# Performance work log

Hardware: AMD Instinct MI355X
Metric: run time of the kernel (lower is better)

The kernel has to match this reference:

```python
import jax, jax.numpy as jnp
import numpy as np

B, S, D, H = 4, 2048, 1024, 16
Dh = D // H


def _layernorm(x, a, b):
    # torch.var default is unbiased (ddof=1)
    mu = jnp.mean(x, axis=-1, keepdims=True)
    sg = jnp.var(x, axis=-1, keepdims=True, ddof=1)
    return (x - mu) / jnp.sqrt(sg + 1e-08) * a + b


def setup_inputs() -> dict:
    key = jax.random.key(0)
    ks = jax.random.split(key, 16)
    s = 1.0 / np.sqrt(D)
    inp = {
        'q': jax.random.normal(ks[0], (B, S, D), jnp.float32),
        'k': jax.random.normal(ks[1], (B, S, D), jnp.float32),
        'v': jax.random.normal(ks[2], (B, S, D), jnp.float32),
        'g': jax.random.normal(ks[3], (B, S, D), jnp.float32),
        # causal mask: True = masked
        'm': jnp.triu(jnp.ones((S, S), jnp.bool_), k=1)[None, None],
        'Wq': jax.random.uniform(ks[4], (D, D), jnp.float32, -s, s),
        'bq': jnp.zeros((D,), jnp.float32),
        'Wk': jax.random.uniform(ks[5], (D, D), jnp.float32, -s, s),
        'bk': jnp.zeros((D,), jnp.float32),
        'Wv': jax.random.uniform(ks[6], (D, D), jnp.float32, -s, s),
        'bv': jnp.zeros((D,), jnp.float32),
        'Wg': jax.random.uniform(ks[7], (D, D), jnp.float32, -s, s),
        'bg': jnp.zeros((D,), jnp.float32),
        'ln_a': jnp.ones((D,), jnp.float32),
        'ln_b': jnp.zeros((D,), jnp.float32),
        'Wo': jax.random.uniform(ks[8], (D, D), jnp.float32, -s, s),
        'bo': jnp.zeros((D,), jnp.float32),
    }
    return inp


def reference(q, k, v, g, m, Wq, bq, Wk, bk, Wv, bv, Wg, bg, ln_a, ln_b, Wo, bo):
    qp = q @ Wq.T + bq
    kp = k @ Wk.T + bk
    vp = v @ Wv.T + bv
    gp = g @ Wg.T + bg
    # gating path: exact GELU (torch default), then custom LayerNorm (unbiased var)
    vp = jax.nn.gelu(vp, approximate=False)
    gp = jax.nn.gelu(gp, approximate=False)
    vp = _layernorm(vp, ln_a, ln_b)
    # [B,S,D] -> [B,H,S,Dh]
    qh = qp.reshape(B, S, H, Dh).transpose(0, 2, 1, 3)
    kh = kp.reshape(B, S, H, Dh).transpose(0, 2, 1, 3)
    vh = vp.reshape(B, S, H, Dh).transpose(0, 2, 1, 3)
    gh = gp.reshape(B, S, H, Dh).transpose(0, 2, 1, 3)
    a = jnp.einsum('bhqd,bhkd->bhqk', qh, kh) / jnp.sqrt(jnp.float32(Dh))
    a = jnp.where(m, -jnp.inf, a)
    a = jax.nn.softmax(a, axis=-1)
    # dropout = 0.0 (inference): no-op
    o = jnp.einsum('bhqk,bhkd->bhqd', a, vh)
    o = o * gh
    o = o.transpose(0, 2, 1, 3).reshape(B, S, D)
    o = o @ Wo.T + bo
    return (o, a)
```

## Files before the change

kernel.cpp:

```cpp
#include <hip/hip_runtime.h>
#include <hip/hip_bf16.h>
#include <cstdint>
#include <cstddef>

#define DEVINL static __device__ __forceinline__

typedef short bf16x8 __attribute__((ext_vector_type(8)));
typedef short s16x4  __attribute__((ext_vector_type(4)));
typedef float f32x4  __attribute__((ext_vector_type(4)));
typedef unsigned short u16;

static constexpr int Bb = 4, Ss = 2048, Dd = 1024, Hh = 16;
static constexpr int Mrows = Bb * Ss;
static constexpr int BHc = Bb * Hh;

DEVINL u16 f2bf(float f) {
    union { float f; uint32_t u; } v; v.f = f;
    uint32_t r = v.u + 0x7fffu + ((v.u >> 16) & 1u);
    return (u16)(r >> 16);
}
DEVINL float bf2f(u16 h) {
    union { uint32_t u; float f; } v; v.u = ((uint32_t)h) << 16;
    return v.f;
}
DEVINL uint32_t cvt_pk_bf16(float lo, float hi) {
    uint32_t r;
    asm("v_cvt_pk_bf16_f32 %0, %1, %2" : "=v"(r) : "v"(lo), "v"(hi));
    return r;
}
DEVINL float gelu_exact(float x) {
    return 0.5f * x * (1.0f + erff(x * 0.70710678118654752f));
}
DEVINL void gload16(const u16* gsrc, u16* ldsdst) {
    auto* g = reinterpret_cast<const __attribute__((address_space(1))) uint32_t*>(
        reinterpret_cast<uintptr_t>(gsrc));
    auto* l = reinterpret_cast<__attribute__((address_space(3))) uint32_t*>(
        reinterpret_cast<uintptr_t>(ldsdst));
    __builtin_amdgcn_global_load_lds(g, l, 16, 0, 0);
}

__global__ __launch_bounds__(256) void k_cvt_in(
    const float* __restrict__ s0, const float* __restrict__ s1,
    const float* __restrict__ s2, const float* __restrict__ s3,
    u16* __restrict__ d0, u16* __restrict__ d1,
    u16* __restrict__ d2, u16* __restrict__ d3, int n4) {
    int t = blockIdx.x * 256 + threadIdx.x;
    if (t >= n4) return;
    const float* s; u16* d;
    switch (blockIdx.y) {
        case 0: s = s0; d = d0; break;
        case 1: s = s1; d = d1; break;
        case 2: s = s2; d = d2; break;
        default: s = s3; d = d3; break;
    }
    float4 v = ((const float4*)s)[t];
    ushort4 o;
    o.x = f2bf(v.x); o.y = f2bf(v.y); o.z = f2bf(v.z); o.w = f2bf(v.w);
    ((ushort4*)d)[t] = o;
}

__global__ __launch_bounds__(256) void k_cvt_w(
    const float* __restrict__ s0, const float* __restrict__ s1,
    const float* __restrict__ s2, const float* __restrict__ s3,
    const float* __restrict__ s4,
    u16* __restrict__ d0, u16* __restrict__ d1, u16* __restrict__ d2,
    u16* __restrict__ d3, u16* __restrict__ d4, int n4) {
    int t = blockIdx.x * 256 + threadIdx.x;
    if (t >= n4) return;
    const float* s; u16* d;
    switch (blockIdx.y) {
        case 0: s = s0; d = d0; break;
        case 1: s = s1; d = d1; break;
        case 2: s = s2; d = d2; break;
        case 3: s = s3; d = d3; break;
        default: s = s4; d = d4; break;
    }
    float4 v = ((const float4*)s)[t];
    ushort4 o;
    o.x = f2bf(v.x); o.y = f2bf(v.y); o.z = f2bf(v.z); o.w = f2bf(v.w);
    ((ushort4*)d)[t] = o;
}

__global__ __launch_bounds__(256, 3) void k_proj(
    const u16* __restrict__ qb, const u16* __restrict__ kb,
    const u16* __restrict__ vb, const u16* __restrict__ gb,
    const u16* __restrict__ Wqb, const u16* __restrict__ Wkb,
    const u16* __restrict__ Wvb, const u16* __restrict__ Wgb,
    const float* __restrict__ bqp, const float* __restrict__ bkp,
    const float* __restrict__ bvp, const float* __restrict__ bgp,
    u16* __restrict__ qp, u16* __restrict__ kpo,
    float* __restrict__ vp, u16* __restrict__ ghb)
{
    __shared__ u16 As[2][128 * 32];
    __shared__ u16 Bs[2][128 * 32];
    const int tid = threadIdx.x, lane = tid & 63, w = tid >> 6;
    const int wm = w >> 1, wn = w & 1;
    const int g = lane >> 4, li = lane & 15;
    const int orig = blockIdx.x;
    const int lid = (orig & 7) * 256 + (orig >> 3);
    const int z = lid >> 9, rem = lid & 511;
    const int m0 = (rem >> 3) * 128, n0 = (rem & 7) * 128;

    const u16 *Ap, *Wp; const float* bias;
    switch (z) {
        case 0: Ap = qb; Wp = Wqb; bias = bqp; break;
        case 1: Ap = kb; Wp = Wkb; bias = bkp; break;
        case 2: Ap = vb; Wp = Wvb; bias = bvp; break;
        default: Ap = gb; Wp = Wgb; bias = bgp; break;
    }

    const int ch0 = (w * 2 + 0) * 64 + lane, ch1 = (w * 2 + 1) * 64 + lane;
    const int row0 = ch0 >> 2, cp0 = ch0 & 3, row1 = ch1 >> 2, cp1 = ch1 & 3;
    const size_t aoff0 = (size_t)(m0 + row0) * 1024 + ((cp0 ^ ((row0 >> 1) & 3)) << 3);
    const size_t aoff1 = (size_t)(m0 + row1) * 1024 + ((cp1 ^ ((row1 >> 1) & 3)) << 3);
    const size_t boff0 = (size_t)(n0 + row0) * 1024 + ((cp0 ^ ((row0 >> 1) & 3)) << 3);
    const size_t boff1 = (size_t)(n0 + row1) * 1024 + ((cp1 ^ ((row1 >> 1) & 3)) << 3);
    const int ldst0 = (w * 2 + 0) * 512, ldst1 = (w * 2 + 1) * 512;

    const f32x4 zero4 = {0.f, 0.f, 0.f, 0.f};
    f32x4 acc[4][4];
#pragma unroll
    for (int m = 0; m < 4; m++)
#pragma unroll
        for (int n = 0; n < 4; n++) acc[m][n] = zero4;

    gload16(Ap + aoff0, &As[0][ldst0]);
    gload16(Ap + aoff1, &As[0][ldst1]);
    gload16(Wp + boff0, &Bs[0][ldst0]);
    gload16(Wp + boff1, &Bs[0][ldst1]);
    __syncthreads();

    for (int kt = 0; kt < 32; ++kt) {
        const int cur = kt & 1;
        if (kt < 31) {
            const int k0n = (kt + 1) * 32;
            gload16(Ap + aoff0 + k0n, &As[cur ^ 1][ldst0]);
            gload16(Ap + aoff1 + k0n, &As[cur ^ 1][ldst1]);
            gload16(Wp + boff0 + k0n, &Bs[cur ^ 1][ldst0]);
            gload16(Wp + boff1 + k0n, &Bs[cur ^ 1][ldst1]);
        }
        bf16x8 af[4], bfr[4];
#pragma unroll
        for (int m = 0; m < 4; m++) {
            int row = wm * 64 + m * 16 + li;
            af[m] = *(const bf16x8*)&As[cur][row * 32 + ((g ^ ((row >> 1) & 3)) << 3)];
        }
#pragma unroll
        for (int n = 0; n < 4; n++) {
            int row = wn * 64 + n * 16 + li;
            bfr[n] = *(const bf16x8*)&Bs[cur][row * 32 + ((g ^ ((row >> 1) & 3)) << 3)];
        }
#pragma unroll
        for (int m = 0; m < 4; m++)
#pragma unroll
            for (int n = 0; n < 4; n++)
                acc[m][n] = __builtin_amdgcn_mfma_f32_16x16x32_bf16(af[m], bfr[n], acc[m][n], 0, 0, 0);
        __syncthreads();
    }

#pragma unroll
    for (int m = 0; m < 4; m++) {
#pragma unroll
        for (int n = 0; n < 4; n++) {
            int col = n0 + wn * 64 + n * 16 + li;
            float bv = bias[col];
#pragma unroll
            for (int r = 0; r < 4; r++) {
                int row = m0 + wm * 64 + m * 16 + g * 4 + r;
                float v = acc[m][n][r] + bv;
                size_t idx = (size_t)row * 1024 + col;
                if (z == 0)      qp[idx]  = f2bf(v * 0.125f);
                else if (z == 1) kpo[idx] = f2bf(v);
                else if (z == 2) vp[idx]  = gelu_exact(v);
                else             ghb[idx] = f2bf(gelu_exact(v));
            }
        }
    }
}

__global__ __launch_bounds__(256, 3) void k_gemm_f(
    const u16* __restrict__ Ap, const u16* __restrict__ Wp,
    const float* __restrict__ bias, float* __restrict__ Cp)
{
    __shared__ u16 As[2][128 * 32];
    __shared__ u16 Bs[2][128 * 32];
    const int tid = threadIdx.x, lane = tid & 63, w = tid >> 6;
    const int wm = w >> 1, wn = w & 1;
    const int g = lane >> 4, li = lane & 15;
    const int orig = blockIdx.x;
    const int lid = (orig & 7) * 64 + (orig >> 3);
    const int m0 = (lid >> 3) * 128, n0 = (lid & 7) * 128;

    const int ch0 = (w * 2 + 0) * 64 + lane, ch1 = (w * 2 + 1) * 64 + lane;
    const int row0 = ch0 >> 2, cp0 = ch0 & 3, row1 = ch1 >> 2, cp1 = ch1 & 3;
    const size_t aoff0 = (size_t)(m0 + row0) * 1024 + ((cp0 ^ ((row0 >> 1) & 3)) << 3);
    const size_t aoff1 = (size_t)(m0 + row1) * 1024 + ((cp1 ^ ((row1 >> 1) & 3)) << 3);
    const size_t boff0 = (size_t)(n0 + row0) * 1024 + ((cp0 ^ ((row0 >> 1) & 3)) << 3);
    const size_t boff1 = (size_t)(n0 + row1) * 1024 + ((cp1 ^ ((row1 >> 1) & 3)) << 3);
    const int ldst0 = (w * 2 + 0) * 512, ldst1 = (w * 2 + 1) * 512;

    const f32x4 zero4 = {0.f, 0.f, 0.f, 0.f};
    f32x4 acc[4][4];
#pragma unroll
    for (int m = 0; m < 4; m++)
#pragma unroll
        for (int n = 0; n < 4; n++) acc[m][n] = zero4;

    gload16(Ap + aoff0, &As[0][ldst0]);
    gload16(Ap + aoff1, &As[0][ldst1]);
    gload16(Wp + boff0, &Bs[0][ldst0]);
    gload16(Wp + boff1, &Bs[0][ldst1]);
    __syncthreads();

    for (int kt = 0; kt < 32; ++kt) {
        const int cur = kt & 1;
        if (kt < 31) {
            const int k0n = (kt + 1) * 32;
            gload16(Ap + aoff0 + k0n, &As[cur ^ 1][ldst0]);
            gload16(Ap + aoff1 + k0n, &As[cur ^ 1][ldst1]);
            gload16(Wp + boff0 + k0n, &Bs[cur ^ 1][ldst0]);
            gload16(Wp + boff1 + k0n, &Bs[cur ^ 1][ldst1]);
        }
        bf16x8 af[4], bfr[4];
#pragma unroll
        for (int m = 0; m < 4; m++) {
            int row = wm * 64 + m * 16 + li;
            af[m] = *(const bf16x8*)&As[cur][row * 32 + ((g ^ ((row >> 1) & 3)) << 3)];
        }
#pragma unroll
        for (int n = 0; n < 4; n++) {
            int row = wn * 64 + n * 16 + li;
            bfr[n] = *(const bf16x8*)&Bs[cur][row * 32 + ((g ^ ((row >> 1) & 3)) << 3)];
        }
#pragma unroll
        for (int m = 0; m < 4; m++)
#pragma unroll
            for (int n = 0; n < 4; n++)
                acc[m][n] = __builtin_amdgcn_mfma_f32_16x16x32_bf16(af[m], bfr[n], acc[m][n], 0, 0, 0);
        __syncthreads();
    }

#pragma unroll
    for (int m = 0; m < 4; m++) {
#pragma unroll
        for (int n = 0; n < 4; n++) {
            int col = n0 + wn * 64 + n * 16 + li;
            float bv = bias[col];
#pragma unroll
            for (int r = 0; r < 4; r++) {
                int row = m0 + wm * 64 + m * 16 + g * 4 + r;
                Cp[(size_t)row * 1024 + col] = acc[m][n][r] + bv;
            }
        }
    }
}

__global__ __launch_bounds__(256) void k_ln(const float* __restrict__ vp,
                                            const float* __restrict__ la,
                                            const float* __restrict__ lb,
                                            u16* __restrict__ vh) {
    int row = blockIdx.x;
    const float* x = vp + (size_t)row * 1024;
    int tid = threadIdx.x;
    float4 v = ((const float4*)x)[tid];
    float s = v.x + v.y + v.z + v.w;
    float s2 = v.x * v.x + v.y * v.y + v.z * v.z + v.w * v.w;
#pragma unroll
    for (int off = 1; off < 64; off <<= 1) {
        s  += __shfl_xor(s, off, 64);
        s2 += __shfl_xor(s2, off, 64);
    }
    __shared__ float red[8];
    int w = tid >> 6, lane = tid & 63;
    if (lane == 0) { red[w] = s; red[4 + w] = s2; }
    __syncthreads();
    s  = red[0] + red[1] + red[2] + red[3];
    s2 = red[4] + red[5] + red[6] + red[7];
    float mu = s * (1.0f / 1024.0f);
    float var = (s2 - 1024.0f * mu * mu) * (1.0f / 1023.0f);
    float rs = rsqrtf(var + 1e-8f);
    float4 a4 = ((const float4*)la)[tid];
    float4 b4 = ((const float4*)lb)[tid];
    ushort4 o;
    o.x = f2bf((v.x - mu) * rs * a4.x + b4.x);
    o.y = f2bf((v.y - mu) * rs * a4.y + b4.y);
    o.z = f2bf((v.z - mu) * rs * a4.z + b4.z);
    o.w = f2bf((v.w - mu) * rs * a4.w + b4.w);
    ((ushort4*)(vh + (size_t)row * 1024))[tid] = o;
}

__global__ __launch_bounds__(256) void k_transpose(const u16* __restrict__ vh,
                                                   u16* __restrict__ vhT) {
    int bh = blockIdx.y, b = bh >> 4, h = bh & 15, s0 = blockIdx.x * 64;
    __shared__ u16 t[64 * 96];
    int tid = threadIdx.x;
#pragma unroll
    for (int j = 0; j < 2; j++) {
        int u = j * 256 + tid;
        int r = u >> 3, c8 = u & 7;
        bf16x8 v = *(const bf16x8*)(vh + ((size_t)(b * 2048 + s0 + r) * 1024 + h * 64 + c8 * 8));
        *(bf16x8*)&t[r * 96 + c8 * 8] = v;
    }
    __syncthreads();
#pragma unroll
    for (int j = 0; j < 2; j++) {
        int u = j * 256 + tid;
        int d = u >> 3, s8 = u & 7;
        bf16x8 vv;
#pragma unroll
        for (int jj = 0; jj < 8; jj++) vv[jj] = (short)t[(s8 * 8 + jj) * 96 + d];
        *(bf16x8*)(vhT + ((size_t)(bh * 64 + d) * 2048 + s0 + s8 * 8)) = vv;
    }
}

__global__ __launch_bounds__(512) void k_attn(const u16* __restrict__ qp,
                                              const u16* __restrict__ kp,
                                              const u16* __restrict__ vhT,
                                              const u16* __restrict__ gh,
                                              float* __restrict__ aout,
                                              u16* __restrict__ gated) {
    __shared__ short Ps[8 * 16 * 128];
    const int tid = threadIdx.x, lane = tid & 63, w = tid >> 6;
    const int g = lane >> 4, li = lane & 15;
    const int orig = blockIdx.x;
    const int lid = (orig & 7) * 64 + (orig >> 3);
    const int bh = lid >> 3, i0 = lid & 7;
    const int b = bh >> 4, h = bh & 15;
    const u16* kbh = kp + ((size_t)(b * 2048) * 1024 + h * 64);
    const u16* vbh = vhT + (size_t)bh * 64 * 2048;
    const u16* ghb_base = gh + (size_t)(b * 2048) * 1024 + h * 64;
    float* arow = aout + (size_t)bh * 2048 * 2048;
    short* Pw = &Ps[w * 2048];
    const f32x4 zero4 = {0.f, 0.f, 0.f, 0.f};

    for (int half = 0; half < 2; ++half) {
        const int bx = half ? (15 - i0) : i0;
        const int q0 = bx * 128;
        const int qrow0 = q0 + w * 16;
        const int qrow = qrow0 + li;
        const u16* qbase = qp + ((size_t)(b * 2048 + qrow) * 1024 + h * 64 + g * 8);
        bf16x8 qa0 = *(const bf16x8*)qbase;
        bf16x8 qa1 = *(const bf16x8*)(qbase + 32);

        for (int kt = bx + 1; kt < 16; ++kt) {
            float* tbase = arow + (size_t)q0 * 2048 + kt * 128;
#pragma unroll
            for (int i = 0; i < 8; i++) {
                int u = i * 512 + tid;
                int row = u >> 5, cu = u & 31;
                __builtin_nontemporal_store(zero4, (f32x4*)(tbase + (size_t)row * 2048 + cu * 4));
            }
        }

        float l_run = 0.f;
        for (int kt = 0; kt <= bx; ++kt) {
            const int k0 = kt * 128;
            const bool full = (kt < bx);
#pragma unroll
            for (int n = 0; n < 8; n++) {
                int rb = k0 + n * 16 + li;
                const u16* krow = kbh + (size_t)rb * 1024 + g * 8;
                bf16x8 kb0 = *(const bf16x8*)krow;
                bf16x8 kb1 = *(const bf16x8*)(krow + 32);
                f32x4 c = zero4;
                c = __builtin_amdgcn_mfma_f32_16x16x32_bf16(kb0, qa0, c, 0, 0, 0);
                c = __builtin_amdgcn_mfma_f32_16x16x32_bf16(kb1, qa1, c, 0, 0, 0);
                if (full) {
#pragma unroll
                    for (int r = 0; r < 4; r++) l_run += __expf(c[r]);
                } else {
#pragma unroll
                    for (int r = 0; r < 4; r++) {
                        int col = k0 + n * 16 + g * 4 + r;
                        l_run += (col <= qrow) ? __expf(c[r]) : 0.0f;
                    }
                }
            }
        }
        l_run += __shfl_xor(l_run, 16, 64);
        l_run += __shfl_xor(l_run, 32, 64);
        const float linv = 1.0f / l_run;

        f32x4 oacc[4];
#pragma unroll
        for (int n = 0; n < 4; n++) oacc[n] = zero4;
        for (int kt = 0; kt <= bx; ++kt) {
            const int k0 = kt * 128;
            const bool full = (kt < bx);
#pragma unroll
            for (int n = 0; n < 8; n++) {
                int rb = k0 + n * 16 + li;
                const u16* krow = kbh + (size_t)rb * 1024 + g * 8;
                bf16x8 kb0 = *(const bf16x8*)krow;
                bf16x8 kb1 = *(const bf16x8*)(krow + 32);
                f32x4 c = zero4;
                c = __builtin_amdgcn_mfma_f32_16x16x32_bf16(kb0, qa0, c, 0, 0, 0);
                c = __builtin_amdgcn_mfma_f32_16x16x32_bf16(kb1, qa1, c, 0, 0, 0);
                if (full) {
#pragma unroll
                    for (int r = 0; r < 4; r++) c[r] = __expf(c[r]) * linv;
                } else {
#pragma unroll
                    for (int r = 0; r < 4; r++) {
                        int col = k0 + n * 16 + g * 4 + r;
                        c[r] = (col <= qrow) ? __expf(c[r]) * linv : 0.0f;
                    }
                }
                __builtin_nontemporal_store(c,
                    (f32x4*)(arow + (size_t)qrow * 2048 + k0 + n * 16 + g * 4));
                uint2 pk;
                pk.x = cvt_pk_bf16(c[0], c[1]);
                pk.y = cvt_pk_bf16(c[2], c[3]);
                int chunk = n * 2 + (g >> 1);
                *(uint2*)&Pw[li * 128 + ((chunk ^ (li & 7)) << 3) + (g & 1) * 4] = pk;
            }
#pragma unroll
            for (int ks = 0; ks < 4; ++ks) {
                int cl = ks * 4 + g;
                bf16x8 pa = *(const bf16x8*)&Pw[li * 128 + ((cl ^ (li & 7)) << 3)];
#pragma unroll
                for (int n = 0; n < 4; n++) {
                    int vr = n * 16 + li;
                    bf16x8 vb = *(const bf16x8*)(vbh + (size_t)vr * 2048 + k0 + cl * 8);
                    oacc[n] = __builtin_amdgcn_mfma_f32_16x16x32_bf16(pa, vb, oacc[n], 0, 0, 0);
                }
            }
        }

#pragma unroll
        for (int n = 0; n < 4; n++) {
            int d8 = n * 2 + (li >> 3), wi = li & 7;
#pragma unroll
            for (int r = 0; r < 4; r++) {
                int lr = g * 4 + r;
                Pw[lr * 64 + ((d8 ^ (lr & 7)) << 3) + wi] = (short)f2bf(oacc[n][r]);
            }
        }
#pragma unroll
        for (int it = 0; it < 2; ++it) {
            int lr = it * 8 + (lane >> 3);
            int c8 = lane & 7;
            int rowq = qrow0 + lr;
            bf16x8 ov = *(const bf16x8*)&Pw[lr * 64 + ((c8 ^ (lr & 7)) << 3)];
            bf16x8 gv = *(const bf16x8*)(ghb_base + (size_t)rowq * 1024 + c8 * 8);
            float p0 = bf2f((u16)ov[0]) * bf2f((u16)gv[0]);
            float p1 = bf2f((u16)ov[1]) * bf2f((u16)gv[1]);
            float p2 = bf2f((u16)ov[2]) * bf2f((u16)gv[2]);
            float p3 = bf2f((u16)ov[3]) * bf2f((u16)gv[3]);
            float p4 = bf2f((u16)ov[4]) * bf2f((u16)gv[4]);
            float p5 = bf2f((u16)ov[5]) * bf2f((u16)gv[5]);
            float p6 = bf2f((u16)ov[6]) * bf2f((u16)gv[6]);
            float p7 = bf2f((u16)ov[7]) * bf2f((u16)gv[7]);
            uint4 outv;
            outv.x = cvt_pk_bf16(p0, p1);
            outv.y = cvt_pk_bf16(p2, p3);
            outv.z = cvt_pk_bf16(p4, p5);
            outv.w = cvt_pk_bf16(p6, p7);
            *(uint4*)(gated + ((size_t)(b * 2048 + rowq)) * 1024 + h * 64 + c8 * 8) = outv;
        }
    }
}

extern "C" void kernel_launch(void* const* d_in, const int* in_sizes, int n_in,
                              void* d_out, int out_size, void* d_ws, size_t ws_size,
                              hipStream_t stream) {
    const float* q  = (const float*)d_in[0];
    const float* k  = (const float*)d_in[1];
    const float* v  = (const float*)d_in[2];
    const float* g  = (const float*)d_in[3];
    const float* Wq = (const float*)d_in[5];
    const float* bq = (const float*)d_in[6];
    const float* Wk = (const float*)d_in[7];
    const float* bk = (const float*)d_in[8];
    const float* Wv = (const float*)d_in[9];
    const float* bv = (const float*)d_in[10];
    const float* Wg = (const float*)d_in[11];
    const float* bg = (const float*)d_in[12];
    const float* ln_a = (const float*)d_in[13];
    const float* ln_b = (const float*)d_in[14];
    const float* Wo = (const float*)d_in[15];
    const float* bo = (const float*)d_in[16];

    float* o_out = (float*)d_out;
    float* a_out = o_out + (size_t)Mrows * Dd;

    u16* qp    = (u16*)d_ws;
    u16* kpb   = qp    + (size_t)Mrows * Dd;
    u16* vhT   = kpb   + (size_t)Mrows * Dd;
    u16* ghb   = vhT   + (size_t)Mrows * Dd;
    u16* gated = ghb   + (size_t)Mrows * Dd;
    u16* Wo_bf = gated + (size_t)Mrows * Dd;

    u16* Wq_bf = (u16*)a_out;
    u16* Wk_bf = Wq_bf + (size_t)Dd * Dd;
    u16* Wv_bf = Wk_bf + (size_t)Dd * Dd;
    u16* Wg_bf = Wv_bf + (size_t)Dd * Dd;
    u16* qb    = Wg_bf + (size_t)Dd * Dd;
    u16* kb2   = qb    + (size_t)Mrows * Dd;
    u16* vb    = kb2   + (size_t)Mrows * Dd;
    u16* gb    = vb    + (size_t)Mrows * Dd;
    float* vp  = (float*)(gb + (size_t)Mrows * Dd);
    u16* vh    = (u16*)(vp + (size_t)Mrows * Dd);

    {
        int n4w = Dd * Dd / 4;
        dim3 gw((n4w + 255) / 256, 5);
        k_cvt_w<<<gw, 256, 0, stream>>>(Wq, Wk, Wv, Wg, Wo,
                                        Wq_bf, Wk_bf, Wv_bf, Wg_bf, Wo_bf, n4w);
        int n4i = Mrows * Dd / 4;
        dim3 gi((n4i + 255) / 256, 4);
        k_cvt_in<<<gi, 256, 0, stream>>>(q, k, v, g, qb, kb2, vb, gb, n4i);
    }

    k_proj<<<2048, 256, 0, stream>>>(qb, kb2, vb, gb,
                                     Wq_bf, Wk_bf, Wv_bf, Wg_bf,
                                     bq, bk, bv, bg,
                                     qp, kpb, vp, ghb);

    k_ln<<<Mrows, 256, 0, stream>>>(vp, ln_a, ln_b, vh);

    dim3 gt(Ss / 64, BHc);
    k_transpose<<<gt, 256, 0, stream>>>(vh, vhT);

    k_attn<<<512, 512, 0, stream>>>(qp, kpb, vhT, ghb, a_out, gated);

    k_gemm_f<<<512, 256, 0, stream>>>(gated, Wo_bf, bo, o_out);
}
```

Baseline: 656.4 us.

## Prefetch two k-tiles ahead in projection GEMMs using explicit vmcnt waits

Both bf16 GEMM kernels (the fused QKVG projection and the output projection) now issue global-to-LDS loads two k-steps ahead instead of one. Explicit s_waitcnt vmcnt(4) lets one tile's loads stay in flight while the current tile is consumed, replacing the full drain at each __syncthreads. This aims to hide global memory latency behind MFMA work. It adds a second barrier per iteration and relies on hand-written waitcnt and barrier asm being correct, without the compiler's own LDS waitcnt handling.

```diff
diff --git a/kernel.cpp b/kernel.cpp
--- a/kernel.cpp
+++ b/kernel.cpp
@@ -124,21 +124,19 @@
 #pragma unroll
         for (int n = 0; n < 4; n++) acc[m][n] = zero4;
 
-    gload16(Ap + aoff0, &As[0][ldst0]);
-    gload16(Ap + aoff1, &As[0][ldst1]);
-    gload16(Wp + boff0, &Bs[0][ldst0]);
-    gload16(Wp + boff1, &Bs[0][ldst1]);
-    __syncthreads();
+    gload16(Ap + aoff0,      &As[0][ldst0]);
+    gload16(Ap + aoff1,      &As[0][ldst1]);
+    gload16(Wp + boff0,      &Bs[0][ldst0]);
+    gload16(Wp + boff1,      &Bs[0][ldst1]);
+    gload16(Ap + aoff0 + 32, &As[1][ldst0]);
+    gload16(Ap + aoff1 + 32, &As[1][ldst1]);
+    gload16(Wp + boff0 + 32, &Bs[1][ldst0]);
+    gload16(Wp + boff1 + 32, &Bs[1][ldst1]);
+    asm volatile("s_waitcnt vmcnt(4)" ::: "memory");
+    asm volatile("s_barrier" ::: "memory");
 
     for (int kt = 0; kt < 32; ++kt) {
         const int cur = kt & 1;
-        if (kt < 31) {
-            const int k0n = (kt + 1) * 32;
-            gload16(Ap + aoff0 + k0n, &As[cur ^ 1][ldst0]);
-            gload16(Ap + aoff1 + k0n, &As[cur ^ 1][ldst1]);
-            gload16(Wp + boff0 + k0n, &Bs[cur ^ 1][ldst0]);
-            gload16(Wp + boff1 + k0n, &Bs[cur ^ 1][ldst1]);
-        }
         bf16x8 af[4], bfr[4];
 #pragma unroll
         for (int m = 0; m < 4; m++) {
@@ -155,7 +153,18 @@
 #pragma unroll
             for (int n = 0; n < 4; n++)
                 acc[m][n] = __builtin_amdgcn_mfma_f32_16x16x32_bf16(af[m], bfr[n], acc[m][n], 0, 0, 0);
-        __syncthreads();
+        asm volatile("s_barrier" ::: "memory");
+        if (kt + 2 < 32) {
+            const int k0n = (kt + 2) * 32;
+            gload16(Ap + aoff0 + k0n, &As[cur][ldst0]);
+            gload16(Ap + aoff1 + k0n, &As[cur][ldst1]);
+            gload16(Wp + boff0 + k0n, &Bs[cur][ldst0]);
+            gload16(Wp + boff1 + k0n, &Bs[cur][ldst1]);
+            asm volatile("s_waitcnt vmcnt(4)" ::: "memory");
+        } else {
+            asm volatile("s_waitcnt vmcnt(0)" ::: "memory");
+        }
+        asm volatile("s_barrier" ::: "memory");
     }
 
 #pragma unroll
@@ -206,21 +215,19 @@
 #pragma unroll
         for (int n = 0; n < 4; n++) acc[m][n] = zero4;
 
-    gload16(Ap + aoff0, &As[0][ldst0]);
-    gload16(Ap + aoff1, &As[0][ldst1]);
-    gload16(Wp + boff0, &Bs[0][ldst0]);
-    gload16(Wp + boff1, &Bs[0][ldst1]);
-    __syncthreads();
+    gload16(Ap + aoff0,      &As[0][ldst0]);
+    gload16(Ap + aoff1,      &As[0][ldst1]);
+    gload16(Wp + boff0,      &Bs[0][ldst0]);
+    gload16(Wp + boff1,      &Bs[0][ldst1]);
+    gload16(Ap + aoff0 + 32, &As[1][ldst0]);
+    gload16(Ap + aoff1 + 32, &As[1][ldst1]);
+    gload16(Wp + boff0 + 32, &Bs[1][ldst0]);
+    gload16(Wp + boff1 + 32, &Bs[1][ldst1]);
+    asm volatile("s_waitcnt vmcnt(4)" ::: "memory");
+    asm volatile("s_barrier" ::: "memory");
 
     for (int kt = 0; kt < 32; ++kt) {
         const int cur = kt & 1;
-        if (kt < 31) {
-            const int k0n = (kt + 1) * 32;
-            gload16(Ap + aoff0 + k0n, &As[cur ^ 1][ldst0]);
-            gload16(Ap + aoff1 + k0n, &As[cur ^ 1][ldst1]);
-            gload16(Wp + boff0 + k0n, &Bs[cur ^ 1][ldst0]);
-            gload16(Wp + boff1 + k0n, &Bs[cur ^ 1][ldst1]);
-        }
         bf16x8 af[4], bfr[4];
 #pragma unroll
         for (int m = 0; m < 4; m++) {
@@ -237,7 +244,18 @@
 #pragma unroll
             for (int n = 0; n < 4; n++)
                 acc[m][n] = __builtin_amdgcn_mfma_f32_16x16x32_bf16(af[m], bfr[n], acc[m][n], 0, 0, 0);
-        __syncthreads();
+        asm volatile("s_barrier" ::: "memory");
+        if (kt + 2 < 32) {
+            const int k0n = (kt + 2) * 32;
+            gload16(Ap + aoff0 + k0n, &As[cur][ldst0]);
+            gload16(Ap + aoff1 + k0n, &As[cur][ldst1]);
+            gload16(Wp + boff0 + k0n, &Bs[cur][ldst0]);
+            gload16(Wp + boff1 + k0n, &Bs[cur][ldst1]);
+            asm volatile("s_waitcnt vmcnt(4)" ::: "memory");
+        } else {
+            asm volatile("s_waitcnt vmcnt(0)" ::: "memory");
+        }
+        asm volatile("s_barrier" ::: "memory");
     }
 
 #pragma unroll
```

New measurement: 648.9 us (median of 3 runs). No clear change (-1.1%).
